# Optimization experiments

Measured on AMD Instinct MI355X. Metric: run time of the kernel, lower is better.

The kernel has to match this reference:

```python
import jax, jax.numpy as jnp
import numpy as np

N = 100000   # nodes
E = 800000   # edges (avg degree 8)
C = 64       # channels
IN_A = 512
IN_V = 512
EPS = 1e-5
BN_SCALE = float(1.0 / np.sqrt(1.0 + EPS))  # eval-mode BN with rm=0, rv=1


def setup_inputs() -> dict:
    key = jax.random.key(0)
    ks = jax.random.split(key, 24)
    s = 0.05
    rnd = lambda k, shp: jax.random.normal(k, shp, jnp.float32)
    inp = {}
    inp["x"] = rnd(ks[0], (N, 2, IN_A))
    inp["edge_index"] = jax.random.randint(ks[1], (2, E), 0, N, dtype=jnp.int32)
    inp["edge_delta"] = jax.random.randint(ks[2], (E,), 0, 30, dtype=jnp.int32)
    inp["edge_self"] = jax.random.randint(ks[3], (E,), 0, 2, dtype=jnp.int32)
    inp["audio_node_mask"] = (jnp.arange(N) % 2) == 0
    # layer_0 linear projections
    inp["W0a"] = rnd(ks[4], (IN_A, C)) * s
    inp["b0a"] = rnd(ks[5], (C,)) * s
    inp["W0v"] = rnd(ks[6], (IN_V, C)) * s
    inp["b0v"] = rnd(ks[7], (C,)) * s
    # batch_0 affine
    inp["bn0_g"] = 1.0 + rnd(ks[8], (C,)) * s
    inp["bn0_b"] = rnd(ks[9], (C,)) * s
    # 4 EdgeConv LinearPathPreact blocks (stacked along leading axis)
    inp["ec_bn1_g"] = 1.0 + rnd(ks[10], (4, 2 * C)) * s
    inp["ec_bn1_b"] = rnd(ks[11], (4, 2 * C)) * s
    inp["ec_fc1_W"] = rnd(ks[12], (4, 2 * C, C)) * s
    inp["ec_bn2_g"] = 1.0 + rnd(ks[13], (4, C)) * s
    inp["ec_bn2_b"] = rnd(ks[14], (4, C)) * s
    inp["ec_fc2_W"] = rnd(ks[15], (4, C, C)) * s
    # batch_1..batch_3 affines
    inp["bn_g"] = 1.0 + rnd(ks[16], (3, C)) * s
    inp["bn_b"] = rnd(ks[17], (3, C)) * s
    # heads
    inp["fca_W"] = rnd(ks[18], (C, 2)) * s
    inp["fca_b"] = rnd(ks[19], (2,)) * s
    inp["fcv_W"] = rnd(ks[20], (C, 2)) * s
    inp["fcv_b"] = rnd(ks[21], (2,)) * s
    inp["fc_W"] = rnd(ks[22], (C, 2)) * s
    inp["fc_b"] = rnd(ks[23], (2,)) * s
    return inp


def _bn(x, g, b):
    # eval-mode BatchNorm1d with running_mean=0, running_var=1
    return x * (BN_SCALE * g) + b


def _lpp(m, g1, b1, W1, g2, b2, W2):
    # LinearPathPreact: BN -> ReLU -> Linear -> BN -> ReLU -> Linear (no biases)
    h = jnp.maximum(_bn(m, g1, b1), 0.0) @ W1
    return jnp.maximum(_bn(h, g2, b2), 0.0) @ W2


def _edgeconv(xf, src, dst, maskf, g1, b1, W1, g2, b2, W2):
    # PyG EdgeConv: message = nn(cat([x_i, x_j - x_i])), mean-aggregated at dst i.
    # Distance-mask is applied as a 0/1 edge weight with masked mean (no dynamic shapes).
    xi = xf[dst]              # [E, C]
    xj = xf[src]              # [E, C]
    msg = _lpp(jnp.concatenate([xi, xj - xi], axis=-1), g1, b1, W1, g2, b2, W2)
    msg = msg * maskf[:, None]
    cnt = jax.ops.segment_sum(maskf, dst, num_segments=N)
    acc = jax.ops.segment_sum(msg, dst, num_segments=N)
    return acc / jnp.maximum(cnt, 1.0)[:, None]


def reference(x, edge_index, edge_delta, edge_self, audio_node_mask,
              W0a, b0a, W0v, b0v, bn0_g, bn0_b,
              ec_bn1_g, ec_bn1_b, ec_fc1_W, ec_bn2_g, ec_bn2_b, ec_fc2_W,
              bn_g, bn_b, fca_W, fca_b, fcv_W, fcv_b, fc_W, fc_b):
    src, dst = edge_index[0], edge_index[1]
    # only the first two distance masks are used in the original forward
    m1 = (edge_delta < 1).astype(x.dtype)
    m2 = (((edge_delta >= 1) & (edge_delta < 4)) | (edge_self == 1)).astype(x.dtype)

    a_out = x[:, 0, :IN_A] @ W0a + b0a
    v_out = x[:, 1, :IN_V] @ W0v + b0v
    gf = jnp.where(audio_node_mask[:, None], a_out, v_out)
    gf = jnp.maximum(_bn(gf, bn0_g, bn0_b), 0.0)

    def block(xin, k):
        p = (ec_bn1_g[k], ec_bn1_b[k], ec_fc1_W[k], ec_bn2_g[k], ec_bn2_b[k], ec_fc2_W[k])
        h = _edgeconv(xin, src, dst, m1, *p)
        return _edgeconv(h, src, dst, m2, *p)

    g1 = jnp.maximum(_bn(block(gf, 0), bn_g[0], bn_b[0]), 0.0)   # dropout is eval-mode identity
    g2 = jnp.maximum(_bn(block(g1, 1) + g1, bn_g[1], bn_b[1]), 0.0)
    g3 = jnp.maximum(_bn(block(g2, 2) + g2, bn_g[2], bn_b[2]), 0.0)
    g4 = block(g3, 3) + g3

    out = g4 @ fc_W + fc_b
    audio_out = gf[audio_node_mask] @ fca_W + fca_b
    video_out = gf[~audio_node_mask] @ fcv_W + fcv_b
    return (out, audio_out, video_out)
```

## Files before the change

kernel.cpp:

```cpp
#include <hip/hip_runtime.h>


#define NN 100000
#define NE 800000
#define NB 391
#define BNS 0.9999950000374998f

typedef __attribute__((ext_vector_type(8))) short short8;
typedef __attribute__((ext_vector_type(4))) float f32x4;

__device__ __forceinline__ float bf_lo(unsigned u){ union{unsigned i; float f;} v; v.i = u << 16; return v.f; }
__device__ __forceinline__ float bf_hi(unsigned u){ union{unsigned i; float f;} v; v.i = u & 0xffff0000u; return v.f; }
__device__ __forceinline__ float bf2f(unsigned short u){ union{unsigned i; float f;} v; v.i = ((unsigned)u) << 16; return v.f; }
__device__ __forceinline__ unsigned short f2bf(float f){
  union{float f; unsigned i;} v; v.f = f;
  unsigned r = v.i + 0x7fffu + ((v.i >> 16) & 1u);
  return (unsigned short)(r >> 16);
}
__device__ __forceinline__ unsigned packbf(float a, float b){
  return (unsigned)f2bf(a) | ((unsigned)f2bf(b) << 16);
}


__global__ __launch_bounds__(256) void hist_kernel(
    const int* __restrict__ ei, const int* __restrict__ edel,
    const int* __restrict__ esel, int* cnt1, int* cnt2)
{
  int e = blockIdx.x * 256 + threadIdx.x;
  if (e >= NE) return;
  int d = edel[e], s = esel[e], dst = ei[NE + e];
  if (d < 1) atomicAdd(cnt1 + dst, 1);
  if ((d >= 1 && d < 4) || s == 1) atomicAdd(cnt2 + dst, 1);
}

__global__ __launch_bounds__(256) void scan1_kernel(
    const int* __restrict__ cnt1, const int* __restrict__ cnt2,
    int* row1, int* row2, int* bsum)
{
  const int a = blockIdx.y;
  const int* cnt = a ? cnt2 : cnt1;
  int* row = a ? row2 : row1;
  int t = threadIdx.x, b = blockIdx.x, i = b * 256 + t;
  int v = (i < NN) ? cnt[i] : 0;
  __shared__ int sc[256];
  sc[t] = v; __syncthreads();
#pragma unroll
  for (int off = 1; off < 256; off <<= 1){
    int x = (t >= off) ? sc[t - off] : 0;
    __syncthreads();
    sc[t] += x;
    __syncthreads();
  }
  if (i < NN) row[i] = sc[t] - v;
  if (t == 255) bsum[a * 400 + b] = sc[t];
}

__global__ __launch_bounds__(512) void scan2_kernel(int* bsum, int* boff, int* ctr)
{
  int t = threadIdx.x;
  __shared__ int sc[512];
  for (int a = 0; a < 2; a++){
    int v = (t < NB) ? bsum[a * 400 + t] : 0;
    __syncthreads();
    sc[t] = v; __syncthreads();
#pragma unroll
    for (int off = 1; off < 512; off <<= 1){
      int x = (t >= off) ? sc[t - off] : 0;
      __syncthreads();
      sc[t] += x;
      __syncthreads();
    }
    if (t < NB) boff[a * 400 + t] = sc[t] - v;
    if (t == NB - 1) ctr[a] = sc[t];
  }
}

__global__ __launch_bounds__(256) void scan3_kernel(
    int* row1, int* row2, int* cur1, int* cur2, const int* __restrict__ boff)
{
  const int a = blockIdx.y;
  int* row = a ? row2 : row1;
  int* cur = a ? cur2 : cur1;
  int i = blockIdx.x * 256 + threadIdx.x;
  if (i >= NN) return;
  int r = row[i] + boff[a * 400 + blockIdx.x];
  row[i] = r;
  cur[i] = r;
}

__global__ __launch_bounds__(256) void inv_kernel(
    const int* __restrict__ cnt1, const int* __restrict__ cnt2,
    float* inv1, float* inv2)
{
  int i = blockIdx.x * 256 + threadIdx.x;
  if (i >= NN) return;
  inv1[i] = 1.f / fmaxf((float)cnt1[i], 1.f);
  inv2[i] = 1.f / fmaxf((float)cnt2[i], 1.f);
}

__global__ __launch_bounds__(256) void compact_kernel(
    const int* __restrict__ ei, const int* __restrict__ edel,
    const int* __restrict__ esel, int* cur1, int* cur2,
    int* s1s, int* s1d, int* s2s, int* s2d)
{
  int e = blockIdx.x * 256 + threadIdx.x;
  if (e >= NE) return;
  int d = edel[e], s = esel[e], src = ei[e], dst = ei[NE + e];
  if (d < 1){ int p = atomicAdd(cur1 + dst, 1); s1s[p] = src; s1d[p] = dst; }
  if ((d >= 1 && d < 4) || s == 1){ int p = atomicAdd(cur2 + dst, 1); s2s[p] = src; s2d[p] = dst; }
}

__global__ __launch_bounds__(256) void prep_w(
    const float* __restrict__ W1, const float* __restrict__ W2,
    const float* __restrict__ g2, unsigned short* __restrict__ wf1,
    unsigned short* __restrict__ wf2)
{
  int g = blockIdx.x * 256 + threadIdx.x;
  if (g >= 6144) return;
  int k = g / 1536, r = g % 1536, f = r >> 6, l = r & 63;
  int q = l >> 4, m = l & 15;
  if (f < 16){
    int t = f >> 2, h = f & 3;
    unsigned short* o = wf1 + (((size_t)k * 16 + f) * 64 + l) * 8;
    const float* Wk = W1 + k * 8192;
    int cp = t * 16 + m;
    float sc = BNS * g2[k * 64 + cp];
#pragma unroll
    for (int j = 0; j < 8; j++){
      int kg = h * 32 + q * 8 + j;
      float w = (kg < 64) ? Wk[(64 + kg) * 64 + cp] : Wk[(kg - 64) * 64 + cp];
      o[j] = f2bf(w * sc);
    }
  } else {
    int f2 = f - 16, t = f2 >> 1, h = f2 & 1;
    unsigned short* o = wf2 + (((size_t)k * 8 + f2) * 64 + l) * 8;
    const float* Wk = W2 + k * 4096;
#pragma unroll
    for (int j = 0; j < 8; j++){
      int kg = h * 32 + q * 8 + j;
      o[j] = f2bf(Wk[kg * 64 + t * 16 + m]);
    }
  }
}

__global__ __launch_bounds__(256) void prep_w0(
    const float* __restrict__ W0a, const float* __restrict__ W0v,
    unsigned short* __restrict__ wf0)
{
  int g = blockIdx.x * 256 + threadIdx.x;
  if (g >= 8192) return;
  int l = g & 63, t = (g >> 6) & 3, ks = (g >> 8) & 15, tt = (g >> 12) & 1;
  const float* W = tt ? W0v : W0a;
  int c = t * 16 + (l & 15);
  int kb = ks * 32 + (l >> 4) * 8;
  unsigned short* o = wf0 + (size_t)g * 8;
#pragma unroll
  for (int j = 0; j < 8; j++) o[j] = f2bf(W[(kb + j) * 64 + c]);
}


__global__ __launch_bounds__(256) void s0_kernel(
    const float* __restrict__ x,
    const float* __restrict__ b0a, const float* __restrict__ b0v,
    const float* __restrict__ bn0g, const float* __restrict__ bn0b,
    const unsigned short* __restrict__ wf0,
    unsigned short* __restrict__ Xb)
{
  const int tt = blockIdx.y;
  const int wv = threadIdx.x >> 6;
  const int l  = threadIdx.x & 63;
  const int q = l >> 4, m16 = l & 15;
  const int wid = blockIdx.x * 4 + wv;
  if (wid >= 3125) return;
  const int node = wid * 16 + m16;
  const float* bias = tt ? b0v : b0a;

  float fs[4][4], ft[4][4];
#pragma unroll
  for (int t = 0; t < 4; t++)
#pragma unroll
    for (int r = 0; r < 4; r++){
      int c = t * 16 + q * 4 + r;
      float s = BNS * bn0g[c];
      fs[t][r] = s;
      ft[t][r] = bias[c] * s + bn0b[c];
    }

  const unsigned short* wbase = wf0 + (size_t)tt * 16 * 4 * 64 * 8;
  const float* xp = x + (size_t)(2 * node + tt) * 1024 + tt * 512 + q * 8;

  f32x4 acc[4];
#pragma unroll
  for (int t = 0; t < 4; t++) acc[t] = (f32x4){0.f, 0.f, 0.f, 0.f};

  for (int ks = 0; ks < 16; ks++){
    float4 xa = *(const float4*)(xp + ks * 32);
    float4 xb = *(const float4*)(xp + ks * 32 + 4);
    union { unsigned u[4]; short8 s; } bb;
    bb.u[0] = packbf(xa.x, xa.y);
    bb.u[1] = packbf(xa.z, xa.w);
    bb.u[2] = packbf(xb.x, xb.y);
    bb.u[3] = packbf(xb.z, xb.w);
    const unsigned short* wk = wbase + (size_t)ks * 4 * 64 * 8 + l * 8;
#pragma unroll
    for (int t = 0; t < 4; t++){
      short8 a = *(const short8*)(wk + t * 64 * 8);
      acc[t] = __builtin_amdgcn_mfma_f32_16x16x32_bf16(a, bb.s, acc[t], 0, 0, 0);
    }
  }

  const int i = 2 * node + tt;
  unsigned short* op = Xb + (size_t)i * 64 + (q << 2);
#pragma unroll
  for (int t = 0; t < 4; t++){
    float v0 = fmaxf(fmaf(acc[t][0], fs[t][0], ft[t][0]), 0.f);
    float v1 = fmaxf(fmaf(acc[t][1], fs[t][1], ft[t][1]), 0.f);
    float v2 = fmaxf(fmaf(acc[t][2], fs[t][2], ft[t][2]), 0.f);
    float v3 = fmaxf(fmaf(acc[t][3], fs[t][3], ft[t][3]), 0.f);
    uint2 w; w.x = packbf(v0, v1); w.y = packbf(v2, v3);
    *(uint2*)(op + t * 16) = w;
  }
}


__global__ __launch_bounds__(256) void msg_pass(
    const unsigned short* __restrict__ fin,
    const int* __restrict__ ssrc, const int* __restrict__ sdst,
    const int* __restrict__ Sp,
    const unsigned short* __restrict__ wf1,
    const float* __restrict__ bn1g, const float* __restrict__ bn1b,
    const float* __restrict__ bn2b,
    unsigned short* __restrict__ msg, int nwaves)
{
  const int l   = threadIdx.x & 63;
  const int wv  = threadIdx.x >> 6;
  const int q   = l >> 4;
  const int m16 = l & 15;
  const int ge  = l >> 2;
  const int gc0 = (l & 3) << 4;

  __shared__ unsigned short r_lds[4][16 * 136];
  unsigned short* rt = &r_lds[wv][0];

  short8 a1[4][4];
#pragma unroll
  for (int t = 0; t < 4; t++)
#pragma unroll
    for (int h = 0; h < 4; h++)
      a1[t][h] = *(const short8*)(wf1 + (((size_t)(t * 4 + h)) * 64 + l) * 8);

  float s1a[16], t1a[16], s1b[16], t1b[16];
#pragma unroll
  for (int j = 0; j < 16; j++){
    s1a[j] = BNS * bn1g[gc0 + j];       t1a[j] = bn1b[gc0 + j];
    s1b[j] = BNS * bn1g[64 + gc0 + j];  t1b[j] = bn1b[64 + gc0 + j];
  }
  f32x4 t2v[4];
#pragma unroll
  for (int t = 0; t < 4; t++)
#pragma unroll
    for (int r = 0; r < 4; r++)
      t2v[t][r] = bn2b[t * 16 + q * 4 + r];

  const int S = *Sp;
  const int nch = (S + 15) >> 4;
  const int wgid = (blockIdx.x << 2) + wv;

  for (int ch = wgid; ch < nch; ch += nwaves){
    int eg = ch * 16 + ge; if (eg > S - 1) eg = S - 1;
    int src = ssrc[eg];
    int dsn = sdst[eg];
    const uint4* ps = (const uint4*)(fin + src * 64 + gc0);
    const uint4* pd = (const uint4*)(fin + dsn * 64 + gc0);
    uint4 su0 = ps[0], su1 = ps[1];
    uint4 du0 = pd[0], du1 = pd[1];

    unsigned sa[8] = {su0.x,su0.y,su0.z,su0.w,su1.x,su1.y,su1.z,su1.w};
    unsigned da[8] = {du0.x,du0.y,du0.z,du0.w,du1.x,du1.y,du1.z,du1.w};
    unsigned rb[8], ra[8];
#pragma unroll
    for (int p = 0; p < 8; p++){
      float fd0 = bf_lo(da[p]), fd1 = bf_hi(da[p]);
      float d0 = bf_lo(sa[p]) - fd0, d1 = bf_hi(sa[p]) - fd1;
      float rb0 = fmaxf(fmaf(d0,  s1b[2*p],   t1b[2*p]),   0.f);
      float rb1 = fmaxf(fmaf(d1,  s1b[2*p+1], t1b[2*p+1]), 0.f);
      float ra0 = fmaxf(fmaf(fd0, s1a[2*p],   t1a[2*p]),   0.f);
      float ra1 = fmaxf(fmaf(fd1, s1a[2*p+1], t1a[2*p+1]), 0.f);
      rb[p] = packbf(rb0, rb1);
      ra[p] = packbf(ra0, ra1);
    }
    unsigned short* wr = rt + ge * 136 + gc0;
    { uint4 u; u.x=rb[0]; u.y=rb[1]; u.z=rb[2]; u.w=rb[3]; *(uint4*)(wr)      = u; }
    { uint4 u; u.x=rb[4]; u.y=rb[5]; u.z=rb[6]; u.w=rb[7]; *(uint4*)(wr + 8)  = u; }
    { uint4 u; u.x=ra[0]; u.y=ra[1]; u.z=ra[2]; u.w=ra[3]; *(uint4*)(wr + 64) = u; }
    { uint4 u; u.x=ra[4]; u.y=ra[5]; u.z=ra[6]; u.w=ra[7]; *(uint4*)(wr + 72) = u; }

    __builtin_amdgcn_wave_barrier();

    const unsigned short* rrow = rt + m16 * 136 + q * 8;
    short8 b1[4];
#pragma unroll
    for (int h = 0; h < 4; h++) b1[h] = *(const short8*)(rrow + h * 32);

    int ee = ch * 16 + m16;
    bool valid = ee < S;
    unsigned short* mp = msg + (size_t)ee * 64 + (q << 2);
#pragma unroll
    for (int t = 0; t < 4; t++){
      f32x4 c = {0.f, 0.f, 0.f, 0.f};
      c = __builtin_amdgcn_mfma_f32_16x16x32_bf16(a1[t][0], b1[0], c, 0, 0, 0);
      c = __builtin_amdgcn_mfma_f32_16x16x32_bf16(a1[t][1], b1[1], c, 0, 0, 0);
      c = __builtin_amdgcn_mfma_f32_16x16x32_bf16(a1[t][2], b1[2], c, 0, 0, 0);
      c = __builtin_amdgcn_mfma_f32_16x16x32_bf16(a1[t][3], b1[3], c, 0, 0, 0);
      if (valid){
        uint2 w;
        w.x = packbf(fmaxf(c[0] + t2v[t][0], 0.f), fmaxf(c[1] + t2v[t][1], 0.f));
        w.y = packbf(fmaxf(c[2] + t2v[t][2], 0.f), fmaxf(c[3] + t2v[t][3], 0.f));
        *(uint2*)(mp + t * 16) = w;
      }
    }
    __builtin_amdgcn_wave_barrier();
  }
}


__global__ __launch_bounds__(256) void aggregate_kernel(
    const unsigned short* __restrict__ msg,
    const int* __restrict__ row, const int* __restrict__ cnt,
    const float* __restrict__ inv,
    const unsigned short* __restrict__ wf2,
    const unsigned short* resid,
    const float* __restrict__ bng, const float* __restrict__ bnb,
    unsigned short* outb, int hasres, int hasbn)
{
  const int l  = threadIdx.x & 63;
  const int wv = threadIdx.x >> 6;
  const int q = l >> 4, m16 = l & 15;
  const int ge = l >> 2, gc0 = (l & 3) << 4;
  const int chunk = (blockIdx.x << 2) + wv;
  if (chunk >= 6250) return;

  __shared__ unsigned short z_lds[4][16 * 72];
  unsigned short* zt = &z_lds[wv][0];

  short8 a2[4][2];
#pragma unroll
  for (int t = 0; t < 4; t++)
#pragma unroll
    for (int h = 0; h < 2; h++)
      a2[t][h] = *(const short8*)(wf2 + (((size_t)(t * 2 + h)) * 64 + l) * 8);

  int d = chunk * 16 + ge;
  int r0 = row[d], deg = cnt[d];
  float s[16];
#pragma unroll
  for (int j = 0; j < 16; j++) s[j] = 0.f;
  const unsigned short* mp = msg + (size_t)r0 * 64 + gc0;
  for (int j = 0; j < deg; j++){
    uint4 u0 = *(const uint4*)(mp);
    uint4 u1 = *(const uint4*)(mp + 8);
    mp += 64;
    unsigned ua[8] = {u0.x,u0.y,u0.z,u0.w,u1.x,u1.y,u1.z,u1.w};
#pragma unroll
    for (int p = 0; p < 8; p++){
      s[2*p]   += bf_lo(ua[p]);
      s[2*p+1] += bf_hi(ua[p]);
    }
  }
  float iv = inv[d];
  unsigned pk[8];
#pragma unroll
  for (int p = 0; p < 8; p++) pk[p] = packbf(s[2*p] * iv, s[2*p+1] * iv);
  unsigned short* wr = zt + ge * 72 + gc0;
  { uint4 u; u.x=pk[0]; u.y=pk[1]; u.z=pk[2]; u.w=pk[3]; *(uint4*)(wr)     = u; }
  { uint4 u; u.x=pk[4]; u.y=pk[5]; u.z=pk[6]; u.w=pk[7]; *(uint4*)(wr + 8) = u; }

  __builtin_amdgcn_wave_barrier();

  const unsigned short* r2row = zt + m16 * 72 + q * 8;
  short8 b2[2];
  b2[0] = *(const short8*)(r2row);
  b2[1] = *(const short8*)(r2row + 32);

  const int dn = chunk * 16 + m16;
  unsigned short* op = outb + (size_t)dn * 64 + (q << 2);
#pragma unroll
  for (int t = 0; t < 4; t++){
    f32x4 c = {0.f, 0.f, 0.f, 0.f};
    c = __builtin_amdgcn_mfma_f32_16x16x32_bf16(a2[t][0], b2[0], c, 0, 0, 0);
    c = __builtin_amdgcn_mfma_f32_16x16x32_bf16(a2[t][1], b2[1], c, 0, 0, 0);
    float v0 = c[0], v1 = c[1], v2 = c[2], v3 = c[3];
    if (hasres){
      uint2 rv = *(const uint2*)(resid + (size_t)dn * 64 + t * 16 + (q << 2));
      v0 += bf_lo(rv.x); v1 += bf_hi(rv.x);
      v2 += bf_lo(rv.y); v3 += bf_hi(rv.y);
    }
    if (hasbn){
      f32x4 g = *(const f32x4*)(bng + t * 16 + (q << 2));
      f32x4 b = *(const f32x4*)(bnb + t * 16 + (q << 2));
      v0 = fmaxf(fmaf(v0, BNS * g[0], b[0]), 0.f);
      v1 = fmaxf(fmaf(v1, BNS * g[1], b[1]), 0.f);
      v2 = fmaxf(fmaf(v2, BNS * g[2], b[2]), 0.f);
      v3 = fmaxf(fmaf(v3, BNS * g[3], b[3]), 0.f);
    }
    uint2 w; w.x = packbf(v0, v1); w.y = packbf(v2, v3);
    *(uint2*)(op + t * 16) = w;
  }
}


__global__ __launch_bounds__(256) void head_final(
    const unsigned short* __restrict__ Xb,
    const float* __restrict__ Wf, const float* __restrict__ bf,
    float* __restrict__ out)
{
  int i = (blockIdx.x << 2) + (threadIdx.x >> 6);
  if (i >= NN) return;
  int l = threadIdx.x & 63;
  float v = bf2f(Xb[i * 64 + l]);
  float2 w = *(const float2*)(Wf + l * 2);
  float p0 = v * w.x, p1 = v * w.y;
#pragma unroll
  for (int off = 32; off; off >>= 1){
    p0 += __shfl_xor(p0, off);
    p1 += __shfl_xor(p1, off);
  }
  if (l == 0){ out[i * 2] = p0 + bf[0]; out[i * 2 + 1] = p1 + bf[1]; }
}

__global__ __launch_bounds__(256) void head_av(
    const unsigned short* __restrict__ Xb,
    const float* __restrict__ Wa, const float* __restrict__ ba,
    const float* __restrict__ Wv, const float* __restrict__ bv,
    float* __restrict__ outA, float* __restrict__ outV)
{
  int i = (blockIdx.x << 2) + (threadIdx.x >> 6);
  if (i >= NN) return;
  int l = threadIdx.x & 63;
  const float* Wf = (i & 1) ? Wv : Wa;
  const float* bb = (i & 1) ? bv : ba;
  float* o = (i & 1) ? (outV + (i >> 1) * 2) : (outA + (i >> 1) * 2);
  float v = bf2f(Xb[i * 64 + l]);
  float2 w = *(const float2*)(Wf + l * 2);
  float p0 = v * w.x, p1 = v * w.y;
#pragma unroll
  for (int off = 32; off; off >>= 1){
    p0 += __shfl_xor(p0, off);
    p1 += __shfl_xor(p1, off);
  }
  if (l == 0){ o[0] = p0 + bb[0]; o[1] = p1 + bb[1]; }
}


extern "C" void kernel_launch(void* const* d_in, const int* in_sizes, int n_in,
                              void* d_out, int out_size, void* d_ws, size_t ws_size,
                              hipStream_t stream)
{
  const float* x    = (const float*)d_in[0];
  const int*   ei   = (const int*)d_in[1];
  const int*   edel = (const int*)d_in[2];
  const int*   esel = (const int*)d_in[3];
  const float* W0a  = (const float*)d_in[5];
  const float* b0a  = (const float*)d_in[6];
  const float* W0v  = (const float*)d_in[7];
  const float* b0v  = (const float*)d_in[8];
  const float* bn0g = (const float*)d_in[9];
  const float* bn0b = (const float*)d_in[10];
  const float* ec1g = (const float*)d_in[11];
  const float* ec1b = (const float*)d_in[12];
  const float* ecW1 = (const float*)d_in[13];
  const float* ec2g = (const float*)d_in[14];
  const float* ec2b = (const float*)d_in[15];
  const float* ecW2 = (const float*)d_in[16];
  const float* bng  = (const float*)d_in[17];
  const float* bnb  = (const float*)d_in[18];
  const float* fcaW = (const float*)d_in[19];
  const float* fcab = (const float*)d_in[20];
  const float* fcvW = (const float*)d_in[21];
  const float* fcvb = (const float*)d_in[22];
  const float* fcW  = (const float*)d_in[23];
  const float* fcb  = (const float*)d_in[24];
  float* out = (float*)d_out;

  char* ws = (char*)d_ws;
  unsigned short* msg  = (unsigned short*)(ws + 0);
  unsigned short* Xb   = (unsigned short*)(ws + 102400000);
  unsigned short* Yb   = (unsigned short*)(ws + 115200000);
  int*            s1s  = (int*)(ws + 128000000);
  int*            s1d  = (int*)(ws + 131200000);
  int*            s2s  = (int*)(ws + 134400000);
  int*            s2d  = (int*)(ws + 137600000);
  int*            cnt1 = (int*)(ws + 140800000);
  int*            cnt2 = (int*)(ws + 141200000);
  int*            row1 = (int*)(ws + 141600000);
  int*            row2 = (int*)(ws + 142000000);
  int*            cur1 = (int*)(ws + 142400000);
  int*            cur2 = (int*)(ws + 142800000);
  float*          inv1 = (float*)(ws + 143200000);
  float*          inv2 = (float*)(ws + 143600000);
  int*            bsum = (int*)(ws + 144000000);
  int*            boff = (int*)(ws + 144003200);
  int*            ctr  = (int*)(ws + 144006400);
  unsigned short* wf1  = (unsigned short*)(ws + 144006464);
  unsigned short* wf2  = (unsigned short*)(ws + 144072000);
  unsigned short* wf0  = (unsigned short*)(ws + 0);

  hipMemsetAsync(cnt1, 0, 800000, stream);

  hist_kernel<<<(NE + 255) / 256, 256, 0, stream>>>(ei, edel, esel, cnt1, cnt2);
  scan1_kernel<<<dim3(NB, 2), 256, 0, stream>>>(cnt1, cnt2, row1, row2, bsum);
  scan2_kernel<<<1, 512, 0, stream>>>(bsum, boff, ctr);
  scan3_kernel<<<dim3(NB, 2), 256, 0, stream>>>(row1, row2, cur1, cur2, boff);
  inv_kernel<<<NB, 256, 0, stream>>>(cnt1, cnt2, inv1, inv2);
  compact_kernel<<<(NE + 255) / 256, 256, 0, stream>>>(ei, edel, esel, cur1, cur2,
                                                       s1s, s1d, s2s, s2d);
  prep_w<<<24, 256, 0, stream>>>(ecW1, ecW2, ec2g, wf1, wf2);
  prep_w0<<<32, 256, 0, stream>>>(W0a, W0v, wf0);

  s0_kernel<<<dim3(782, 2), 256, 0, stream>>>(x, b0a, b0v, bn0g, bn0b, wf0, Xb);
  head_av<<<25000, 256, 0, stream>>>(Xb, fcaW, fcab, fcvW, fcvb,
                                     out + 2 * NN, out + 2 * NN + 100000);

  const int EB = 1024;
  const int nwaves = EB * 4;
  const int AGB = 1563;

  for (int k = 0; k < 4; k++){
    const unsigned short* w1k = wf1 + (size_t)k * 16 * 64 * 8;
    const unsigned short* w2k = wf2 + (size_t)k * 8 * 64 * 8;
    const float* g1p = ec1g + k * 128;
    const float* b1p = ec1b + k * 128;
    const float* b2p = ec2b + k * 64;

    msg_pass<<<EB, 256, 0, stream>>>(Xb, s1s, s1d, ctr + 0, w1k,
                                     g1p, b1p, b2p, msg, nwaves);
    aggregate_kernel<<<AGB, 256, 0, stream>>>(msg, row1, cnt1, inv1, w2k,
                                              nullptr, nullptr, nullptr,
                                              Yb, 0, 0);
    msg_pass<<<EB, 256, 0, stream>>>(Yb, s2s, s2d, ctr + 1, w1k,
                                     g1p, b1p, b2p, msg, nwaves);
    const unsigned short* resid = (k == 0) ? nullptr : Xb;
    const float* bg = (k < 3) ? (bng + k * 64) : nullptr;
    const float* bb = (k < 3) ? (bnb + k * 64) : nullptr;
    aggregate_kernel<<<AGB, 256, 0, stream>>>(msg, row2, cnt2, inv2, w2k,
                                              resid, bg, bb,
                                              Xb, (k == 0) ? 0 : 1, (k < 3) ? 1 : 0);
  }

  head_final<<<25000, 256, 0, stream>>>(Xb, fcW, fcb, out);
}
```

Baseline: 967.7 us.

## Fuse edge message MLP with per-destination aggregation, dropping the message buffer

Replaces the separate msg_pass and aggregate kernels with one edge_pass kernel. Each wave owns 16 destination nodes, walks their CSR edge range, computes the per-edge MLP with MFMA and accumulates the results directly from LDS. This removes the global write and re-read of the 800K×64 bf16 message buffer. It also packs dst&15 into the src index so the destination features come from LDS, and folds the first BN scale into the weights so the prologue only adds a bias. The costs are that wave work now follows node degree, which can be imbalanced, and that folding by dividing by g1 assumes g1 is positive and nonzero.

Result: faster. 940.0 us (-2.9%).

```diff
diff --git a/kernel.cpp b/kernel.cpp
--- a/kernel.cpp
+++ b/kernel.cpp
@@ -101,22 +101,31 @@
 __global__ __launch_bounds__(256) void compact_kernel(
     const int* __restrict__ ei, const int* __restrict__ edel,
     const int* __restrict__ esel, int* cur1, int* cur2,
-    int* s1s, int* s1d, int* s2s, int* s2d)
+    int* s1s, int* s2s)
 {
   int e = blockIdx.x * 256 + threadIdx.x;
   if (e >= NE) return;
   int d = edel[e], s = esel[e], src = ei[e], dst = ei[NE + e];
-  if (d < 1){ int p = atomicAdd(cur1 + dst, 1); s1s[p] = src; s1d[p] = dst; }
-  if ((d >= 1 && d < 4) || s == 1){ int p = atomicAdd(cur2 + dst, 1); s2s[p] = src; s2d[p] = dst; }
+  int rec = src | ((dst & 15) << 20);
+  if (d < 1){ int p = atomicAdd(cur1 + dst, 1); s1s[p] = rec; }
+  if ((d >= 1 && d < 4) || s == 1){ int p = atomicAdd(cur2 + dst, 1); s2s[p] = rec; }
 }
 
 __global__ __launch_bounds__(256) void prep_w(
     const float* __restrict__ W1, const float* __restrict__ W2,
-    const float* __restrict__ g2, unsigned short* __restrict__ wf1,
-    unsigned short* __restrict__ wf2)
+    const float* __restrict__ g1, const float* __restrict__ g2,
+    const float* __restrict__ b1,
+    unsigned short* __restrict__ wf1, unsigned short* __restrict__ wf2,
+    float* __restrict__ t1p)
 {
   int g = blockIdx.x * 256 + threadIdx.x;
-  if (g >= 6144) return;
+  if (g >= 6656) return;
+  if (g >= 6144){
+    int i = g - 6144;
+    int k = i >> 7, c = i & 127;
+    t1p[i] = b1[k * 128 + c] / (BNS * g1[k * 128 + c]);
+    return;
+  }
   int k = g / 1536, r = g % 1536, f = r >> 6, l = r & 63;
   int q = l >> 4, m = l & 15;
   if (f < 16){
@@ -124,12 +133,19 @@
     unsigned short* o = wf1 + (((size_t)k * 16 + f) * 64 + l) * 8;
     const float* Wk = W1 + k * 8192;
     int cp = t * 16 + m;
-    float sc = BNS * g2[k * 64 + cp];
+    float cs = BNS * g2[k * 64 + cp];
 #pragma unroll
     for (int j = 0; j < 8; j++){
       int kg = h * 32 + q * 8 + j;
-      float w = (kg < 64) ? Wk[(64 + kg) * 64 + cp] : Wk[(kg - 64) * 64 + cp];
-      o[j] = f2bf(w * sc);
+      float w, rs;
+      if (kg < 64){
+        w  = Wk[(64 + kg) * 64 + cp];
+        rs = BNS * g1[k * 128 + 64 + kg];
+      } else {
+        w  = Wk[(kg - 64) * 64 + cp];
+        rs = BNS * g1[k * 128 + kg - 64];
+      }
+      o[j] = f2bf(w * rs * cs);
     }
   } else {
     int f2 = f - 16, t = f2 >> 1, h = f2 & 1;
@@ -223,77 +239,104 @@
 }
 
 
-__global__ __launch_bounds__(256) void msg_pass(
+__global__ __launch_bounds__(256, 3) void edge_pass(
     const unsigned short* __restrict__ fin,
-    const int* __restrict__ ssrc, const int* __restrict__ sdst,
-    const int* __restrict__ Sp,
+    const int* __restrict__ spk,
+    const int* __restrict__ row, const int* __restrict__ cnt,
+    const float* __restrict__ inv,
     const unsigned short* __restrict__ wf1,
-    const float* __restrict__ bn1g, const float* __restrict__ bn1b,
+    const unsigned short* __restrict__ wf2,
+    const float* __restrict__ t1p,
     const float* __restrict__ bn2b,
-    unsigned short* __restrict__ msg, int nwaves)
-{
-  const int l   = threadIdx.x & 63;
-  const int wv  = threadIdx.x >> 6;
-  const int q   = l >> 4;
-  const int m16 = l & 15;
-  const int ge  = l >> 2;
-  const int gc0 = (l & 3) << 4;
-
-  __shared__ unsigned short r_lds[4][16 * 136];
-  unsigned short* rt = &r_lds[wv][0];
-
-  short8 a1[4][4];
+    const unsigned short* resid,
+    const float* __restrict__ bng, const float* __restrict__ bnb,
+    unsigned short* __restrict__ outb, int hasres, int hasbn)
+{
+  const int tid = threadIdx.x;
+  const int l = tid & 63;
+  const int wv = tid >> 6;
+  const int q = l >> 4, m16 = l & 15;
+  const int ge = l >> 2, gc0 = (l & 3) << 4;
+
+  __shared__ unsigned short wlds[8192];
+  __shared__ unsigned short rt_s[4][16 * 136];
+  __shared__ unsigned short zt_s[4][16 * 72];
+  __shared__ unsigned short xi_s[4][16 * 72];
+
+  {
+    const uint4* s4 = (const uint4*)wf1;
+    uint4* d4 = (uint4*)wlds;
+#pragma unroll
+    for (int i = 0; i < 4; i++) d4[tid + 256 * i] = s4[tid + 256 * i];
+  }
+  __syncthreads();
+
+  int chunk = blockIdx.x * 4 + wv;
+  const bool active = chunk < 6250;
+  if (chunk > 6249) chunk = 6249;
+  const int d0 = chunk << 4;
+  const int nd = d0 + ge;
+
+  unsigned short* rt = rt_s[wv];
+  unsigned short* zt = zt_s[wv];
+  unsigned short* xi = xi_s[wv];
+
+  const int rlo = row[nd], deg = cnt[nd];
+  const float ivd = inv[nd];
+
+  float t1a[16], t1b[16];
+#pragma unroll
+  for (int j0 = 0; j0 < 16; j0 += 4){
+    *(float4*)(t1a + j0) = *(const float4*)(t1p + gc0 + j0);
+    *(float4*)(t1b + j0) = *(const float4*)(t1p + 64 + gc0 + j0);
+  }
+  f32x4 t2v[4];
 #pragma unroll
   for (int t = 0; t < 4; t++)
-#pragma unroll
-    for (int h = 0; h < 4; h++)
-      a1[t][h] = *(const short8*)(wf1 + (((size_t)(t * 4 + h)) * 64 + l) * 8);
-
-  float s1a[16], t1a[16], s1b[16], t1b[16];
-#pragma unroll
-  for (int j = 0; j < 16; j++){
-    s1a[j] = BNS * bn1g[gc0 + j];       t1a[j] = bn1b[gc0 + j];
-    s1b[j] = BNS * bn1g[64 + gc0 + j];  t1b[j] = bn1b[64 + gc0 + j];
-  }
-  f32x4 t2v[4];
-#pragma unroll
-  for (int t = 0; t < 4; t++)
-#pragma unroll
-    for (int r = 0; r < 4; r++)
-      t2v[t][r] = bn2b[t * 16 + q * 4 + r];
-
-  const int S = *Sp;
-  const int nch = (S + 15) >> 4;
-  const int wgid = (blockIdx.x << 2) + wv;
-
-  for (int ch = wgid; ch < nch; ch += nwaves){
-    int eg = ch * 16 + ge; if (eg > S - 1) eg = S - 1;
-    int src = ssrc[eg];
-    int dsn = sdst[eg];
-    const uint4* ps = (const uint4*)(fin + src * 64 + gc0);
-    const uint4* pd = (const uint4*)(fin + dsn * 64 + gc0);
+    t2v[t] = *(const f32x4*)(bn2b + t * 16 + (q << 2));
+
+  {
+    const uint4* px = (const uint4*)(fin + (size_t)nd * 64 + gc0);
+    uint4 u0 = px[0], u1 = px[1];
+    unsigned short* wr = xi + ge * 72 + gc0;
+    *(uint4*)(wr)     = u0;
+    *(uint4*)(wr + 8) = u1;
+  }
+
+  const int r_begin = __shfl(rlo, 0);
+  const int r_end   = __shfl(rlo + deg, 63);
+
+  float s[16];
+#pragma unroll
+  for (int j = 0; j < 16; j++) s[j] = 0.f;
+
+  __builtin_amdgcn_wave_barrier();
+
+  for (int e0 = r_begin; e0 < r_end; e0 += 16){
+    int eg = e0 + ge; if (eg >= r_end) eg = r_end - 1;
+    unsigned v = (unsigned)spk[eg];
+    int src = v & 0xFFFFF;
+    int d15 = (v >> 20) & 15;
+    const uint4* ps = (const uint4*)(fin + (size_t)src * 64 + gc0);
     uint4 su0 = ps[0], su1 = ps[1];
-    uint4 du0 = pd[0], du1 = pd[1];
+    const uint4* pxi = (const uint4*)(xi + d15 * 72 + gc0);
+    uint4 xu0 = pxi[0], xu1 = pxi[1];
 
     unsigned sa[8] = {su0.x,su0.y,su0.z,su0.w,su1.x,su1.y,su1.z,su1.w};
-    unsigned da[8] = {du0.x,du0.y,du0.z,du0.w,du1.x,du1.y,du1.z,du1.w};
-    unsigned rb[8], ra[8];
+    unsigned xa[8] = {xu0.x,xu0.y,xu0.z,xu0.w,xu1.x,xu1.y,xu1.z,xu1.w};
+    unsigned rb[8], rc[8];
 #pragma unroll
     for (int p = 0; p < 8; p++){
-      float fd0 = bf_lo(da[p]), fd1 = bf_hi(da[p]);
-      float d0 = bf_lo(sa[p]) - fd0, d1 = bf_hi(sa[p]) - fd1;
-      float rb0 = fmaxf(fmaf(d0,  s1b[2*p],   t1b[2*p]),   0.f);
-      float rb1 = fmaxf(fmaf(d1,  s1b[2*p+1], t1b[2*p+1]), 0.f);
-      float ra0 = fmaxf(fmaf(fd0, s1a[2*p],   t1a[2*p]),   0.f);
-      float ra1 = fmaxf(fmaf(fd1, s1a[2*p+1], t1a[2*p+1]), 0.f);
-      rb[p] = packbf(rb0, rb1);
-      ra[p] = packbf(ra0, ra1);
+      float x0 = bf_lo(xa[p]), x1 = bf_hi(xa[p]);
+      float e0f = bf_lo(sa[p]) - x0, e1f = bf_hi(sa[p]) - x1;
+      rb[p] = packbf(fmaxf(e0f + t1b[2*p], 0.f), fmaxf(e1f + t1b[2*p+1], 0.f));
+      rc[p] = packbf(fmaxf(x0 + t1a[2*p], 0.f),  fmaxf(x1 + t1a[2*p+1], 0.f));
     }
     unsigned short* wr = rt + ge * 136 + gc0;
     { uint4 u; u.x=rb[0]; u.y=rb[1]; u.z=rb[2]; u.w=rb[3]; *(uint4*)(wr)      = u; }
     { uint4 u; u.x=rb[4]; u.y=rb[5]; u.z=rb[6]; u.w=rb[7]; *(uint4*)(wr + 8)  = u; }
-    { uint4 u; u.x=ra[0]; u.y=ra[1]; u.z=ra[2]; u.w=ra[3]; *(uint4*)(wr + 64) = u; }
-    { uint4 u; u.x=ra[4]; u.y=ra[5]; u.z=ra[6]; u.w=ra[7]; *(uint4*)(wr + 72) = u; }
+    { uint4 u; u.x=rc[0]; u.y=rc[1]; u.z=rc[2]; u.w=rc[3]; *(uint4*)(wr + 64) = u; }
+    { uint4 u; u.x=rc[4]; u.y=rc[5]; u.z=rc[6]; u.w=rc[7]; *(uint4*)(wr + 72) = u; }
 
     __builtin_amdgcn_wave_barrier();
 
@@ -302,87 +345,59 @@
 #pragma unroll
     for (int h = 0; h < 4; h++) b1[h] = *(const short8*)(rrow + h * 32);
 
-    int ee = ch * 16 + m16;
-    bool valid = ee < S;
-    unsigned short* mp = msg + (size_t)ee * 64 + (q << 2);
 #pragma unroll
     for (int t = 0; t < 4; t++){
       f32x4 c = {0.f, 0.f, 0.f, 0.f};
-      c = __builtin_amdgcn_mfma_f32_16x16x32_bf16(a1[t][0], b1[0], c, 0, 0, 0);
-      c = __builtin_amdgcn_mfma_f32_16x16x32_bf16(a1[t][1], b1[1], c, 0, 0, 0);
-      c = __builtin_amdgcn_mfma_f32_16x16x32_bf16(a1[t][2], b1[2], c, 0, 0, 0);
-      c = __builtin_amdgcn_mfma_f32_16x16x32_bf16(a1[t][3], b1[3], c, 0, 0, 0);
-      if (valid){
-        uint2 w;
-        w.x = packbf(fmaxf(c[0] + t2v[t][0], 0.f), fmaxf(c[1] + t2v[t][1], 0.f));
-        w.y = packbf(fmaxf(c[2] + t2v[t][2], 0.f), fmaxf(c[3] + t2v[t][3], 0.f));
-        *(uint2*)(mp + t * 16) = w;
+#pragma unroll
+      for (int h = 0; h < 4; h++){
+        short8 a = *(const short8*)(wlds + ((t * 4 + h) * 64 + l) * 8);
+        c = __builtin_amdgcn_mfma_f32_16x16x32_bf16(a, b1[h], c, 0, 0, 0);
       }
-    }
+      uint2 w;
+      w.x = packbf(fmaxf(c[0] + t2v[t][0], 0.f), fmaxf(c[1] + t2v[t][1], 0.f));
+      w.y = packbf(fmaxf(c[2] + t2v[t][2], 0.f), fmaxf(c[3] + t2v[t][3], 0.f));
+      *(uint2*)(zt + m16 * 72 + t * 16 + (q << 2)) = w;
+    }
+
     __builtin_amdgcn_wave_barrier();
-  }
-}
-
-
-__global__ __launch_bounds__(256) void aggregate_kernel(
-    const unsigned short* __restrict__ msg,
-    const int* __restrict__ row, const int* __restrict__ cnt,
-    const float* __restrict__ inv,
-    const unsigned short* __restrict__ wf2,
-    const unsigned short* resid,
-    const float* __restrict__ bng, const float* __restrict__ bnb,
-    unsigned short* outb, int hasres, int hasbn)
-{
-  const int l  = threadIdx.x & 63;
-  const int wv = threadIdx.x >> 6;
-  const int q = l >> 4, m16 = l & 15;
-  const int ge = l >> 2, gc0 = (l & 3) << 4;
-  const int chunk = (blockIdx.x << 2) + wv;
-  if (chunk >= 6250) return;
-
-  __shared__ unsigned short z_lds[4][16 * 72];
-  unsigned short* zt = &z_lds[wv][0];
-
-  short8 a2[4][2];
-#pragma unroll
-  for (int t = 0; t < 4; t++)
-#pragma unroll
-    for (int h = 0; h < 2; h++)
-      a2[t][h] = *(const short8*)(wf2 + (((size_t)(t * 2 + h)) * 64 + l) * 8);
-
-  int d = chunk * 16 + ge;
-  int r0 = row[d], deg = cnt[d];
-  float s[16];
-#pragma unroll
-  for (int j = 0; j < 16; j++) s[j] = 0.f;
-  const unsigned short* mp = msg + (size_t)r0 * 64 + gc0;
-  for (int j = 0; j < deg; j++){
-    uint4 u0 = *(const uint4*)(mp);
-    uint4 u1 = *(const uint4*)(mp + 8);
-    mp += 64;
-    unsigned ua[8] = {u0.x,u0.y,u0.z,u0.w,u1.x,u1.y,u1.z,u1.w};
-#pragma unroll
-    for (int p = 0; p < 8; p++){
-      s[2*p]   += bf_lo(ua[p]);
-      s[2*p+1] += bf_hi(ua[p]);
-    }
-  }
-  float iv = inv[d];
+
+    int jlo = rlo - e0;       if (jlo < 0)  jlo = 0;
+    int jhi = rlo + deg - e0; if (jhi > 16) jhi = 16;
+    for (int j = jlo; j < jhi; j++){
+      const uint4* pz = (const uint4*)(zt + j * 72 + gc0);
+      uint4 z0 = pz[0], z1 = pz[1];
+      unsigned za[8] = {z0.x,z0.y,z0.z,z0.w,z1.x,z1.y,z1.z,z1.w};
+#pragma unroll
+      for (int p = 0; p < 8; p++){
+        s[2*p]   += bf_lo(za[p]);
+        s[2*p+1] += bf_hi(za[p]);
+      }
+    }
+    __builtin_amdgcn_wave_barrier();
+  }
+
   unsigned pk[8];
 #pragma unroll
-  for (int p = 0; p < 8; p++) pk[p] = packbf(s[2*p] * iv, s[2*p+1] * iv);
+  for (int p = 0; p < 8; p++) pk[p] = packbf(s[2*p] * ivd, s[2*p+1] * ivd);
   unsigned short* wr = zt + ge * 72 + gc0;
   { uint4 u; u.x=pk[0]; u.y=pk[1]; u.z=pk[2]; u.w=pk[3]; *(uint4*)(wr)     = u; }
   { uint4 u; u.x=pk[4]; u.y=pk[5]; u.z=pk[6]; u.w=pk[7]; *(uint4*)(wr + 8) = u; }
 
   __builtin_amdgcn_wave_barrier();
+
+  short8 a2[4][2];
+#pragma unroll
+  for (int t = 0; t < 4; t++)
+#pragma unroll
+    for (int h = 0; h < 2; h++)
+      a2[t][h] = *(const short8*)(wf2 + (((size_t)(t * 2 + h)) * 64 + l) * 8);
 
   const unsigned short* r2row = zt + m16 * 72 + q * 8;
   short8 b2[2];
   b2[0] = *(const short8*)(r2row);
   b2[1] = *(const short8*)(r2row + 32);
 
-  const int dn = chunk * 16 + m16;
+  const int dn = d0 + m16;
   unsigned short* op = outb + (size_t)dn * 64 + (q << 2);
 #pragma unroll
   for (int t = 0; t < 4; t++){
@@ -403,8 +418,10 @@
       v2 = fmaxf(fmaf(v2, BNS * g[2], b[2]), 0.f);
       v3 = fmaxf(fmaf(v3, BNS * g[3], b[3]), 0.f);
     }
-    uint2 w; w.x = packbf(v0, v1); w.y = packbf(v2, v3);
-    *(uint2*)(op + t * 16) = w;
+    if (active){
+      uint2 w; w.x = packbf(v0, v1); w.y = packbf(v2, v3);
+      *(uint2*)(op + t * 16) = w;
+    }
   }
 }
 
@@ -483,13 +500,10 @@
   float* out = (float*)d_out;
 
   char* ws = (char*)d_ws;
-  unsigned short* msg  = (unsigned short*)(ws + 0);
   unsigned short* Xb   = (unsigned short*)(ws + 102400000);
   unsigned short* Yb   = (unsigned short*)(ws + 115200000);
   int*            s1s  = (int*)(ws + 128000000);
-  int*            s1d  = (int*)(ws + 131200000);
   int*            s2s  = (int*)(ws + 134400000);
-  int*            s2d  = (int*)(ws + 137600000);
   int*            cnt1 = (int*)(ws + 140800000);
   int*            cnt2 = (int*)(ws + 141200000);
   int*            row1 = (int*)(ws + 141600000);
@@ -502,7 +516,8 @@
   int*            boff = (int*)(ws + 144003200);
   int*            ctr  = (int*)(ws + 144006400);
   unsigned short* wf1  = (unsigned short*)(ws + 144006464);
-  unsigned short* wf2  = (unsigned short*)(ws + 144072000);
+  unsigned short* wf2  = (unsigned short*)(ws + 144137536);
+  float*          t1p  = (float*)(ws + 144203072);
   unsigned short* wf0  = (unsigned short*)(ws + 0);
 
   hipMemsetAsync(cnt1, 0, 800000, stream);
@@ -513,38 +528,31 @@
   scan3_kernel<<<dim3(NB, 2), 256, 0, stream>>>(row1, row2, cur1, cur2, boff);
   inv_kernel<<<NB, 256, 0, stream>>>(cnt1, cnt2, inv1, inv2);
   compact_kernel<<<(NE + 255) / 256, 256, 0, stream>>>(ei, edel, esel, cur1, cur2,
-                                                       s1s, s1d, s2s, s2d);
-  prep_w<<<24, 256, 0, stream>>>(ecW1, ecW2, ec2g, wf1, wf2);
+                                                       s1s, s2s);
+  prep_w<<<26, 256, 0, stream>>>(ecW1, ecW2, ec1g, ec2g, ec1b, wf1, wf2, t1p);
   prep_w0<<<32, 256, 0, stream>>>(W0a, W0v, wf0);
 
   s0_kernel<<<dim3(782, 2), 256, 0, stream>>>(x, b0a, b0v, bn0g, bn0b, wf0, Xb);
   head_av<<<25000, 256, 0, stream>>>(Xb, fcaW, fcab, fcvW, fcvb,
                                      out + 2 * NN, out + 2 * NN + 100000);
 
-  const int EB = 1024;
-  const int nwaves = EB * 4;
-  const int AGB = 1563;
+  const int EGB = 1563;
 
   for (int k = 0; k < 4; k++){
     const unsigned short* w1k = wf1 + (size_t)k * 16 * 64 * 8;
     const unsigned short* w2k = wf2 + (size_t)k * 8 * 64 * 8;
-    const float* g1p = ec1g + k * 128;
-    const float* b1p = ec1b + k * 128;
+    const float* t1k = t1p + k * 128;
     const float* b2p = ec2b + k * 64;
 
-    msg_pass<<<EB, 256, 0, stream>>>(Xb, s1s, s1d, ctr + 0, w1k,
-                                     g1p, b1p, b2p, msg, nwaves);
-    aggregate_kernel<<<AGB, 256, 0, stream>>>(msg, row1, cnt1, inv1, w2k,
-                                              nullptr, nullptr, nullptr,
-                                              Yb, 0, 0);
-    msg_pass<<<EB, 256, 0, stream>>>(Yb, s2s, s2d, ctr + 1, w1k,
-                                     g1p, b1p, b2p, msg, nwaves);
+    edge_pass<<<EGB, 256, 0, stream>>>(Xb, s1s, row1, cnt1, inv1, w1k, w2k,
+                                       t1k, b2p, nullptr, nullptr, nullptr,
+                                       Yb, 0, 0);
     const unsigned short* resid = (k == 0) ? nullptr : Xb;
     const float* bg = (k < 3) ? (bng + k * 64) : nullptr;
     const float* bb = (k < 3) ? (bnb + k * 64) : nullptr;
-    aggregate_kernel<<<AGB, 256, 0, stream>>>(msg, row2, cnt2, inv2, w2k,
-                                              resid, bg, bb,
-                                              Xb, (k == 0) ? 0 : 1, (k < 3) ? 1 : 0);
+    edge_pass<<<EGB, 256, 0, stream>>>(Yb, s2s, row2, cnt2, inv2, w1k, w2k,
+                                       t1k, b2p, resid, bg, bb,
+                                       Xb, (k == 0) ? 0 : 1, (k < 3) ? 1 : 0);
   }
 
   head_final<<<25000, 256, 0, stream>>>(Xb, fcW, fcb, out);
```
